# Performance work log

Measured on AMD Instinct MI355X. Metric: run time of the kernel, lower is better.

Reference implementation:

```python
import jax, jax.numpy as jnp
import numpy as np

CLASSES = 21  # from init_kwargs
EPS = 1e-8


def setup_inputs() -> dict:
    key = jax.random.key(0)
    k1, k2 = jax.random.split(key)
    img = jax.random.normal(k1, (8, 128, 256, 256), dtype=jnp.float32)
    gt = jax.random.randint(k2, (8, 1, 256, 256), 0, CLASSES, dtype=jnp.int32)
    return {"img": img, "gt": gt}


def reference(img, gt):
    # img: [B, C, H, W] float; gt: [B, 1, H, W] int labels in [0, CLASSES)
    # The torch loop replaces every pixel of class i with the per-(image,channel)
    # mean of img over pixels of class i. Since class masks are disjoint, this is
    # a single segment-mean + gather.
    B, C, H, W = img.shape
    HW = H * W
    labels = gt.reshape(B, HW)                                   # [B, HW]
    seg = (jnp.arange(B, dtype=labels.dtype)[:, None] * CLASSES + labels).reshape(-1)  # [B*HW]
    data = img.transpose(0, 2, 3, 1).reshape(B * HW, C)          # [B*HW, C]
    sums = jax.ops.segment_sum(data, seg, num_segments=B * CLASSES)          # [B*CLASSES, C]
    counts = jax.ops.segment_sum(jnp.ones((B * HW,), img.dtype), seg,
                                 num_segments=B * CLASSES)                   # [B*CLASSES]
    means = sums / (counts[:, None] + EPS)                       # [B*CLASSES, C]
    out = means[seg].reshape(B, H, W, C).transpose(0, 3, 1, 2)   # [B, C, H, W]
    # Pixels with out-of-range labels (none here) would be untouched by the loop.
    valid = (gt >= 0) & (gt < CLASSES)                           # [B,1,H,W]
    return jnp.where(valid, out, img)
```

## Files before the change

kernel.cpp:

```cpp
#include <hip/hip_runtime.h>
#include <hip/hip_bf16.h>

#define BATCH 8
#define CHAN 128
#define CLASSES 21
#define HW 65536
#define PIX_CHUNKS 4
#define CHUNK (HW / PIX_CHUNKS)
#define EPS 1e-8f
#define STRIDE 257

struct U8x4 { unsigned char x, y, z, w; };

template <typename L>
__device__ __forceinline__ int4 loadLabels4(const L* __restrict__ p, int i);

template <>
__device__ __forceinline__ int4 loadLabels4<int>(const int* __restrict__ p, int i) {
    return ((const int4*)p)[i];
}
template <>
__device__ __forceinline__ int4 loadLabels4<unsigned char>(const unsigned char* __restrict__ p, int i) {
    U8x4 g = ((const U8x4*)p)[i];
    return make_int4(g.x, g.y, g.z, g.w);
}

__global__ __launch_bounds__(256) void k_pack_count(
    const int* __restrict__ gt, unsigned char* __restrict__ packed,
    int* __restrict__ counts) {
    __shared__ int lc[CLASSES];
    const int t = threadIdx.x;
    const int b = blockIdx.y;
    const size_t base = (size_t)b * HW + (size_t)blockIdx.x * 1024;
    if (t < CLASSES) lc[t] = 0;
    __syncthreads();
    int4 g = ((const int4*)(gt + base))[t];
    if (packed) {
        U8x4 pk;
        pk.x = (unsigned char)g.x; pk.y = (unsigned char)g.y;
        pk.z = (unsigned char)g.z; pk.w = (unsigned char)g.w;
        ((U8x4*)(packed + base))[t] = pk;
    }
    atomicAdd(&lc[g.x], 1); atomicAdd(&lc[g.y], 1);
    atomicAdd(&lc[g.z], 1); atomicAdd(&lc[g.w], 1);
    __syncthreads();
    if (t < CLASSES) atomicAdd(&counts[b * CLASSES + t], lc[t]);
}

template <typename L>
__global__ __launch_bounds__(256) void k_reduce(
    const float* __restrict__ img, const L* __restrict__ gt,
    float* __restrict__ sums) {
    __shared__ float acc[CLASSES * STRIDE];
    const int t = threadIdx.x;
    const int chunk = blockIdx.x;
    const int c = blockIdx.y;
    const int b = blockIdx.z;

    #pragma unroll
    for (int cls = 0; cls < CLASSES; ++cls) acc[cls * STRIDE + t] = 0.0f;
    __syncthreads();

    const float4* __restrict__ imgp =
        (const float4*)(img + ((size_t)(b * CHAN + c)) * HW + (size_t)chunk * CHUNK);
    const L* __restrict__ gtp = gt + (size_t)b * HW + (size_t)chunk * CHUNK;
    float* __restrict__ accT = acc + t;

    #pragma unroll 4
    for (int i = t; i < CHUNK / 4; i += 256) {
        float4 v = imgp[i];
        int4 g = loadLabels4<L>(gtp, i);
        accT[g.x * STRIDE] += v.x;
        accT[g.y * STRIDE] += v.y;
        accT[g.z * STRIDE] += v.z;
        accT[g.w * STRIDE] += v.w;
    }
    __syncthreads();

    for (int off = 128; off >= 1; off >>= 1) {
        if (t < off) {
            #pragma unroll
            for (int cls = 0; cls < CLASSES; ++cls)
                acc[cls * STRIDE + t] += acc[cls * STRIDE + t + off];
        }
        __syncthreads();
    }

    if (t < CLASSES)
        unsafeAtomicAdd(&sums[((size_t)b * CLASSES + t) * CHAN + c], acc[t * STRIDE]);
}

__global__ __launch_bounds__(256) void k_means(
    const float* __restrict__ sums, const int* __restrict__ counts,
    float* __restrict__ means) {
    int i = blockIdx.x * 256 + threadIdx.x;
    if (i < BATCH * CLASSES * CHAN)
        means[i] = sums[i] / ((float)counts[i / CHAN] + EPS);
}

template <typename L>
__global__ __launch_bounds__(256) void k_gather(
    const L* __restrict__ gt, const float* __restrict__ means,
    float* __restrict__ out) {
    __shared__ float m[CLASSES];
    const int t = threadIdx.x;
    const int chunk = blockIdx.x;
    const int c = blockIdx.y;
    const int b = blockIdx.z;
    if (t < CLASSES) m[t] = means[((size_t)b * CLASSES + t) * CHAN + c];
    __syncthreads();

    const L* __restrict__ gtp = gt + (size_t)b * HW + (size_t)chunk * CHUNK;
    float4* __restrict__ outp =
        (float4*)(out + ((size_t)(b * CHAN + c)) * HW + (size_t)chunk * CHUNK);

    #pragma unroll 4
    for (int i = t; i < CHUNK / 4; i += 256) {
        int4 g = loadLabels4<L>(gtp, i);
        float4 o;
        o.x = m[g.x];
        o.y = m[g.y];
        o.z = m[g.z];
        o.w = m[g.w];
        outp[i] = o;
    }
}

extern "C" void kernel_launch(void* const* d_in, const int* in_sizes, int n_in,
                              void* d_out, int out_size, void* d_ws, size_t ws_size,
                              hipStream_t stream) {
    const float* img = (const float*)d_in[0];
    const int* gt = (const int*)d_in[1];
    float* out = (float*)d_out;

    size_t off = 0;
    float* sums = (float*)d_ws;
    off += (size_t)BATCH * CLASSES * CHAN * sizeof(float);
    int* counts = (int*)((char*)d_ws + off);
    off += (size_t)BATCH * CLASSES * sizeof(int);
    float* means = (float*)((char*)d_ws + off);
    off += (size_t)BATCH * CLASSES * CHAN * sizeof(float);
    off = (off + 255) & ~(size_t)255;
    unsigned char* packed = (unsigned char*)d_ws + off;
    const bool usePacked = (ws_size >= off + (size_t)BATCH * HW);

    size_t zero_bytes = (size_t)BATCH * CLASSES * CHAN * sizeof(float)
                      + (size_t)BATCH * CLASSES * sizeof(int);
    hipMemsetAsync(d_ws, 0, zero_bytes, stream);

    dim3 gPack(HW / 1024, BATCH);
    k_pack_count<<<gPack, 256, 0, stream>>>(gt, usePacked ? packed : nullptr, counts);

    dim3 grid(PIX_CHUNKS, CHAN, BATCH);
    if (usePacked)
        k_reduce<unsigned char><<<grid, 256, 0, stream>>>(img, packed, sums);
    else
        k_reduce<int><<<grid, 256, 0, stream>>>(img, gt, sums);

    k_means<<<(BATCH * CLASSES * CHAN + 255) / 256, 256, 0, stream>>>(sums, counts, means);

    if (usePacked)
        k_gather<unsigned char><<<grid, 256, 0, stream>>>(packed, means, out);
    else
        k_gather<int><<<grid, 256, 0, stream>>>(gt, means, out);
}
```

Before: 461.9 us.

## Use lane-privatized LDS atomics, shuffle reductions, and 4-channel gather blocks

The reduce kernel drops the per-thread 21x257 LDS accumulator and its tree reduction. It uses a 21x64 per-lane array updated with LDS float atomics, then a wavefront shuffle reduction. Counting uses the same per-lane scheme. The gather kernel now writes four channels per block from one label read, which cuts label traffic. The int-label fallback path is removed, so the workspace is assumed to hold the packed labels, and four waves sharing a lane slot now contend on LDS atomics.

```diff
diff --git a/kernel.cpp b/kernel.cpp
--- a/kernel.cpp
+++ b/kernel.cpp
@@ -5,89 +5,80 @@
 #define CHAN 128
 #define CLASSES 21
 #define HW 65536
-#define PIX_CHUNKS 4
-#define CHUNK (HW / PIX_CHUNKS)
 #define EPS 1e-8f
-#define STRIDE 257
-
-struct U8x4 { unsigned char x, y, z, w; };
-
-template <typename L>
-__device__ __forceinline__ int4 loadLabels4(const L* __restrict__ p, int i);
-
-template <>
-__device__ __forceinline__ int4 loadLabels4<int>(const int* __restrict__ p, int i) {
-    return ((const int4*)p)[i];
-}
-template <>
-__device__ __forceinline__ int4 loadLabels4<unsigned char>(const unsigned char* __restrict__ p, int i) {
-    U8x4 g = ((const U8x4*)p)[i];
-    return make_int4(g.x, g.y, g.z, g.w);
-}
 
 __global__ __launch_bounds__(256) void k_pack_count(
     const int* __restrict__ gt, unsigned char* __restrict__ packed,
     int* __restrict__ counts) {
-    __shared__ int lc[CLASSES];
+    __shared__ int lc[CLASSES * 64];
     const int t = threadIdx.x;
+    const int lane = t & 63;
     const int b = blockIdx.y;
     const size_t base = (size_t)b * HW + (size_t)blockIdx.x * 1024;
-    if (t < CLASSES) lc[t] = 0;
+
+    for (int i = t; i < CLASSES * 64; i += 256) lc[i] = 0;
     __syncthreads();
+
     int4 g = ((const int4*)(gt + base))[t];
-    if (packed) {
-        U8x4 pk;
-        pk.x = (unsigned char)g.x; pk.y = (unsigned char)g.y;
-        pk.z = (unsigned char)g.z; pk.w = (unsigned char)g.w;
-        ((U8x4*)(packed + base))[t] = pk;
+    uchar4 pk = make_uchar4((unsigned char)g.x, (unsigned char)g.y,
+                            (unsigned char)g.z, (unsigned char)g.w);
+    ((uchar4*)(packed + base))[t] = pk;
+    atomicAdd(&lc[g.x * 64 + lane], 1);
+    atomicAdd(&lc[g.y * 64 + lane], 1);
+    atomicAdd(&lc[g.z * 64 + lane], 1);
+    atomicAdd(&lc[g.w * 64 + lane], 1);
+    __syncthreads();
+
+    if (t < 64) {
+        #pragma unroll
+        for (int cls = 0; cls < CLASSES; ++cls) {
+            int s = lc[cls * 64 + t];
+            #pragma unroll
+            for (int off = 32; off >= 1; off >>= 1) s += __shfl_xor(s, off, 64);
+            if (t == 0) atomicAdd(&counts[b * CLASSES + cls], s);
+        }
     }
-    atomicAdd(&lc[g.x], 1); atomicAdd(&lc[g.y], 1);
-    atomicAdd(&lc[g.z], 1); atomicAdd(&lc[g.w], 1);
-    __syncthreads();
-    if (t < CLASSES) atomicAdd(&counts[b * CLASSES + t], lc[t]);
 }
 
-template <typename L>
 __global__ __launch_bounds__(256) void k_reduce(
-    const float* __restrict__ img, const L* __restrict__ gt,
+    const float* __restrict__ img, const unsigned char* __restrict__ packed,
     float* __restrict__ sums) {
-    __shared__ float acc[CLASSES * STRIDE];
+    __shared__ float acc[CLASSES * 64];
     const int t = threadIdx.x;
+    const int lane = t & 63;
     const int chunk = blockIdx.x;
     const int c = blockIdx.y;
     const int b = blockIdx.z;
 
-    #pragma unroll
-    for (int cls = 0; cls < CLASSES; ++cls) acc[cls * STRIDE + t] = 0.0f;
+    for (int i = t; i < CLASSES * 64; i += 256) acc[i] = 0.0f;
     __syncthreads();
 
     const float4* __restrict__ imgp =
-        (const float4*)(img + ((size_t)(b * CHAN + c)) * HW + (size_t)chunk * CHUNK);
-    const L* __restrict__ gtp = gt + (size_t)b * HW + (size_t)chunk * CHUNK;
-    float* __restrict__ accT = acc + t;
+        (const float4*)(img + ((size_t)(b * CHAN + c)) * HW + (size_t)chunk * (HW / 4));
+    const uchar4* __restrict__ gtp =
+        (const uchar4*)(packed + (size_t)b * HW + (size_t)chunk * (HW / 4));
 
     #pragma unroll 4
-    for (int i = t; i < CHUNK / 4; i += 256) {
+    for (int i = t; i < (HW / 4) / 4; i += 256) {
         float4 v = imgp[i];
-        int4 g = loadLabels4<L>(gtp, i);
-        accT[g.x * STRIDE] += v.x;
-        accT[g.y * STRIDE] += v.y;
-        accT[g.z * STRIDE] += v.z;
-        accT[g.w * STRIDE] += v.w;
+        uchar4 g = gtp[i];
+        unsafeAtomicAdd(&acc[(int)g.x * 64 + lane], v.x);
+        unsafeAtomicAdd(&acc[(int)g.y * 64 + lane], v.y);
+        unsafeAtomicAdd(&acc[(int)g.z * 64 + lane], v.z);
+        unsafeAtomicAdd(&acc[(int)g.w * 64 + lane], v.w);
     }
     __syncthreads();
 
-    for (int off = 128; off >= 1; off >>= 1) {
-        if (t < off) {
+    if (t < 64) {
+        #pragma unroll
+        for (int cls = 0; cls < CLASSES; ++cls) {
+            float s = acc[cls * 64 + t];
             #pragma unroll
-            for (int cls = 0; cls < CLASSES; ++cls)
-                acc[cls * STRIDE + t] += acc[cls * STRIDE + t + off];
+            for (int off = 32; off >= 1; off >>= 1) s += __shfl_xor(s, off, 64);
+            if (t == 0)
+                unsafeAtomicAdd(&sums[((size_t)b * CLASSES + cls) * CHAN + c], s);
         }
-        __syncthreads();
     }
-
-    if (t < CLASSES)
-        unsafeAtomicAdd(&sums[((size_t)b * CLASSES + t) * CHAN + c], acc[t * STRIDE]);
 }
 
 __global__ __launch_bounds__(256) void k_means(
@@ -98,31 +89,38 @@
         means[i] = sums[i] / ((float)counts[i / CHAN] + EPS);
 }
 
-template <typename L>
 __global__ __launch_bounds__(256) void k_gather(
-    const L* __restrict__ gt, const float* __restrict__ means,
+    const unsigned char* __restrict__ packed, const float* __restrict__ means,
     float* __restrict__ out) {
-    __shared__ float m[CLASSES];
+    __shared__ float4 m4[CLASSES];
     const int t = threadIdx.x;
     const int chunk = blockIdx.x;
-    const int c = blockIdx.y;
+    const int c0 = blockIdx.y * 4;
     const int b = blockIdx.z;
-    if (t < CLASSES) m[t] = means[((size_t)b * CLASSES + t) * CHAN + c];
+    const int PIX = HW / 16;
+
+    if (t < CLASSES * 4) {
+        int cls = t >> 2, j = t & 3;
+        ((float*)m4)[t] = means[((size_t)b * CLASSES + cls) * CHAN + c0 + j];
+    }
     __syncthreads();
 
-    const L* __restrict__ gtp = gt + (size_t)b * HW + (size_t)chunk * CHUNK;
-    float4* __restrict__ outp =
-        (float4*)(out + ((size_t)(b * CHAN + c)) * HW + (size_t)chunk * CHUNK);
+    const uchar4* __restrict__ gtp =
+        (const uchar4*)(packed + (size_t)b * HW + (size_t)chunk * PIX);
+    float* __restrict__ outbase =
+        out + ((size_t)(b * CHAN + c0)) * HW + (size_t)chunk * PIX;
 
-    #pragma unroll 4
-    for (int i = t; i < CHUNK / 4; i += 256) {
-        int4 g = loadLabels4<L>(gtp, i);
-        float4 o;
-        o.x = m[g.x];
-        o.y = m[g.y];
-        o.z = m[g.z];
-        o.w = m[g.w];
-        outp[i] = o;
+    for (int i = t; i < PIX / 4; i += 256) {
+        uchar4 g = gtp[i];
+        float4 mx = m4[g.x], my = m4[g.y], mz = m4[g.z], mw = m4[g.w];
+        float4 o0 = make_float4(mx.x, my.x, mz.x, mw.x);
+        float4 o1 = make_float4(mx.y, my.y, mz.y, mw.y);
+        float4 o2 = make_float4(mx.z, my.z, mz.z, mw.z);
+        float4 o3 = make_float4(mx.w, my.w, mz.w, mw.w);
+        ((float4*)(outbase          ))[i] = o0;
+        ((float4*)(outbase +     HW))[i] = o1;
+        ((float4*)(outbase + 2 * HW))[i] = o2;
+        ((float4*)(outbase + 3 * HW))[i] = o3;
     }
 }
 
@@ -142,25 +140,19 @@
     off += (size_t)BATCH * CLASSES * CHAN * sizeof(float);
     off = (off + 255) & ~(size_t)255;
     unsigned char* packed = (unsigned char*)d_ws + off;
-    const bool usePacked = (ws_size >= off + (size_t)BATCH * HW);
 
     size_t zero_bytes = (size_t)BATCH * CLASSES * CHAN * sizeof(float)
                       + (size_t)BATCH * CLASSES * sizeof(int);
     hipMemsetAsync(d_ws, 0, zero_bytes, stream);
 
     dim3 gPack(HW / 1024, BATCH);
-    k_pack_count<<<gPack, 256, 0, stream>>>(gt, usePacked ? packed : nullptr, counts);
+    k_pack_count<<<gPack, 256, 0, stream>>>(gt, packed, counts);
 
-    dim3 grid(PIX_CHUNKS, CHAN, BATCH);
-    if (usePacked)
-        k_reduce<unsigned char><<<grid, 256, 0, stream>>>(img, packed, sums);
-    else
-        k_reduce<int><<<grid, 256, 0, stream>>>(img, gt, sums);
+    dim3 gRed(4, CHAN, BATCH);
+    k_reduce<<<gRed, 256, 0, stream>>>(img, packed, sums);
 
     k_means<<<(BATCH * CLASSES * CHAN + 255) / 256, 256, 0, stream>>>(sums, counts, means);
 
-    if (usePacked)
-        k_gather<unsigned char><<<grid, 256, 0, stream>>>(packed, means, out);
-    else
-        k_gather<int><<<grid, 256, 0, stream>>>(gt, means, out);
+    dim3 gGat(16, CHAN / 4, BATCH);
+    k_gather<<<gGat, 256, 0, stream>>>(packed, means, out);
 }
```

Result: slower. 718.1 us (+55.5%).
